# Kernel tuning notes

Measured on AMD Instinct MI355X. Metric: run time of the kernel, lower is better.

Reference implementation:

```python
import jax, jax.numpy as jnp
import numpy as np

N_NODES = 100000
N_EDGES = 640000
LATDIM = 128
GNN_LAYER = 3
LN_EPS = 1e-5


def setup_inputs() -> dict:
    key = jax.random.key(0)
    k1, k2, k3, k4 = jax.random.split(key, 4)
    embeds = jax.random.normal(k1, (N_NODES, LATDIM), dtype=jnp.float32)
    adj_row = jax.random.randint(k2, (N_EDGES,), 0, N_NODES, dtype=jnp.int32)
    adj_col = jax.random.randint(k3, (N_EDGES,), 0, N_NODES, dtype=jnp.int32)
    adj_val = jax.random.uniform(k4, (N_EDGES,), dtype=jnp.float32)
    return {"embeds": embeds, "adj_row": adj_row, "adj_col": adj_col, "adj_val": adj_val}


def _layer_norm(x):
    # nn.LayerNorm(latdim, elementwise_affine=False)
    mu = jnp.mean(x, axis=-1, keepdims=True)
    var = jnp.mean(jnp.square(x - mu), axis=-1, keepdims=True)
    return (x - mu) / jnp.sqrt(var + LN_EPS)


def _spmm(adj_row, adj_col, adj_val, x):
    # out[r] += val * x[c] for each edge (r, c, val)  -- sparse [N,N] @ [N,d]
    msgs = adj_val[:, None] * x[adj_col]  # [E, d]
    return jax.ops.segment_sum(msgs, adj_row, num_segments=N_NODES)


def reference(embeds, adj_row, adj_col, adj_val):
    x = _layer_norm(embeds)
    acc = jnp.zeros_like(x)  # gnn_layer > 0, so hop-0 embeds are NOT included
    for _ in range(GNN_LAYER):
        x = _spmm(adj_row, adj_col, adj_val, x)
        acc = acc + x
    return acc
```

## Files before the change

kernel.cpp:

```cpp
#include <hip/hip_runtime.h>

#define N_NODES 100000
#define N_EDGES 640000
#define LATDIM  128
#define LN_EPS  1e-5f

typedef unsigned int u32;
typedef float f32x4 __attribute__((ext_vector_type(4)));

#define SCAN_NB   98
#define N_PAD     (SCAN_NB * 1024)

#define LN_BLOCKS   (N_NODES / 8)
#define HIST_BLOCKS ((N_EDGES + 255) / 256)

#define APP_K      7
#define APP_EDGES  (256 * APP_K)
#define APP_NB     ((N_EDGES + APP_EDGES - 1) / APP_EDGES)

__device__ __forceinline__ float bflo(u32 u) { return __uint_as_float(u << 16); }
__device__ __forceinline__ float bfhi(u32 u) { return __uint_as_float(u & 0xffff0000u); }
__device__ __forceinline__ u32 pack_bf2(float a, float b) {
    u32 ua = __float_as_uint(a), ub = __float_as_uint(b);
    ua = (ua + 0x7fffu + ((ua >> 16) & 1u)) >> 16;
    ub = (ub + 0x7fffu + ((ub >> 16) & 1u)) >> 16;
    return ua | (ub << 16);
}

__device__ __forceinline__ u32 pack_edge(int col, float val) {
    u32 q = (u32)fminf(val * 32768.0f + 0.5f, 32767.0f);
    return (u32)col | (q << 17);
}
__device__ __forceinline__ int   edge_col(u32 r) { return (int)(r & 0x1FFFFu); }
__device__ __forceinline__ float edge_val(u32 r) { return (float)(r >> 17) * (1.0f / 32768.0f); }

__global__ __launch_bounds__(256) void ln_hist_kernel(const float* __restrict__ in,
                                                      u32* __restrict__ out,
                                                      const int* __restrict__ rowi,
                                                      int* __restrict__ cnt) {
    int b = blockIdx.x;
    if (b < LN_BLOCKS) {
        int tid  = threadIdx.x;
        int wave = tid >> 6;
        int lane = tid & 63;
        int half = lane >> 5;
        int sub  = lane & 31;
        int row  = b * 8 + wave * 2 + half;
        f32x4 v = __builtin_nontemporal_load(((const f32x4*)in) + (size_t)row * 32 + sub);
        float s  = v.x + v.y + v.z + v.w;
        float ss = v.x * v.x + v.y * v.y + v.z * v.z + v.w * v.w;
        #pragma unroll
        for (int o = 16; o > 0; o >>= 1) {
            s  += __shfl_xor(s,  o, 64);
            ss += __shfl_xor(ss, o, 64);
        }
        float mu   = s * (1.0f / LATDIM);
        float var  = ss * (1.0f / LATDIM) - mu * mu;
        float rstd = rsqrtf(var + LN_EPS);
        uint2 w;
        w.x = pack_bf2((v.x - mu) * rstd, (v.y - mu) * rstd);
        w.y = pack_bf2((v.z - mu) * rstd, (v.w - mu) * rstd);
        ((uint2*)out)[(size_t)row * 32 + sub] = w;
    } else {
        int e = (b - LN_BLOCKS) * 256 + threadIdx.x;
        if (e < N_EDGES) atomicAdd(&cnt[rowi[e]], 1);
    }
}

__global__ __launch_bounds__(256) void scan_a_kernel(int* __restrict__ cnt,
                                                     int* __restrict__ csums) {
    __shared__ int ts[256];
    int t = threadIdx.x;
    int base = blockIdx.x * 1024 + t * 4;
    int4 v = *(const int4*)(cnt + base);
    int s = v.x + v.y + v.z + v.w;
    ts[t] = s;
    __syncthreads();
    #pragma unroll
    for (int o = 1; o < 256; o <<= 1) {
        int u = 0;
        if (t >= o) u = ts[t - o];
        __syncthreads();
        if (t >= o) ts[t] += u;
        __syncthreads();
    }
    int excl = ts[t] - s;
    int4 w;
    w.x = excl;
    w.y = excl + v.x;
    w.z = excl + v.x + v.y;
    w.w = excl + v.x + v.y + v.z;
    *(int4*)(cnt + base) = w;
    if (t == 255) csums[blockIdx.x] = ts[255];
}

__global__ __launch_bounds__(128) void scan_b_kernel(const int* __restrict__ csums,
                                                     int* __restrict__ bsums,
                                                     int* __restrict__ gcur) {
    __shared__ int ss[128];
    int t = threadIdx.x;
    int own = (t < SCAN_NB) ? csums[t] : 0;
    ss[t] = own;
    __syncthreads();
    #pragma unroll
    for (int o = 1; o < 128; o <<= 1) {
        int u = 0;
        if (t >= o) u = ss[t - o];
        __syncthreads();
        if (t >= o) ss[t] += u;
        __syncthreads();
    }
    if (t < SCAN_NB) {
        int off = ss[t] - own;
        bsums[t] = off;
        gcur[t]  = off;
    }
    if (t == SCAN_NB) bsums[SCAN_NB] = N_EDGES;
}

__global__ __launch_bounds__(256) void bucket_append_kernel(const int* __restrict__ rowi,
                                                            const int* __restrict__ coli,
                                                            const float* __restrict__ vali,
                                                            int* __restrict__ gcur,
                                                            uint2* __restrict__ staging) {
    __shared__ int hist[SCAN_NB];
    __shared__ int base[SCAN_NB];
    int t = threadIdx.x;
    if (t < SCAN_NB) hist[t] = 0;
    __syncthreads();
    int e0 = blockIdx.x * APP_EDGES;
    int r[APP_K]; int c[APP_K]; float v[APP_K]; int bk[APP_K];
    #pragma unroll
    for (int k = 0; k < APP_K; ++k) {
        int e = e0 + k * 256 + t;
        if (e < N_EDGES) {
            r[k] = rowi[e]; c[k] = coli[e]; v[k] = vali[e];
            bk[k] = r[k] >> 10;
            atomicAdd(&hist[bk[k]], 1);
        } else {
            bk[k] = -1;
        }
    }
    __syncthreads();
    if (t < SCAN_NB) {
        int h = hist[t];
        base[t] = h ? atomicAdd(&gcur[t], h) : 0;
        hist[t] = 0;
    }
    __syncthreads();
    #pragma unroll
    for (int k = 0; k < APP_K; ++k) {
        if (bk[k] >= 0) {
            int idx = atomicAdd(&hist[bk[k]], 1);
            staging[base[bk[k]] + idx] =
                make_uint2(((u32)(r[k] & 1023) << 17) | (u32)c[k],
                           __float_as_uint(v[k]));
        }
    }
}

__global__ __launch_bounds__(256) void fine_scatter_kernel(const int* __restrict__ cnt,
                                                           const int* __restrict__ bsums,
                                                           const uint2* __restrict__ staging,
                                                           u32* __restrict__ recs) {
    __shared__ int cur[1024];
    int b = blockIdx.x, t = threadIdx.x;
    *(int4*)&cur[t * 4] = *(const int4*)&cnt[b * 1024 + t * 4];
    __syncthreads();
    int gbase = bsums[b];
    int n = bsums[b + 1] - gbase;
    for (int i = t; i < n; i += 256) {
        uint2 s = staging[gbase + i];
        int rowLocal = (int)(s.x >> 17);
        int col = (int)(s.x & 0x1FFFFu);
        int pos = gbase + atomicAdd(&cur[rowLocal], 1);
        recs[pos] = pack_edge(col, __uint_as_float(s.y));
    }
}

__global__ __launch_bounds__(256) void spmm_csr_kernel(const int* __restrict__ cnt,
                                                       const int* __restrict__ bsums,
                                                       const u32* __restrict__ recs,
                                                       const u32* __restrict__ x,
                                                       u32* __restrict__ y,
                                                       const u32* __restrict__ add0,
                                                       const u32* __restrict__ add1,
                                                       float* __restrict__ out,
                                                       int mode) {
    int tid  = threadIdx.x;
    int wave = tid >> 6;
    int lane = tid & 63;
    int row  = blockIdx.x * 16 + wave * 4 + (lane >> 4);
    int sub  = lane & 15;
    int e   = cnt[row]     + bsums[row >> 10];
    int end = cnt[row + 1] + bsums[(row + 1) >> 10];
    const uint4* x4 = (const uint4*)x;
    float a0=0,a1=0,a2=0,a3=0,a4=0,a5=0,a6=0,a7=0;
    for (; e + 4 <= end; e += 4) {
        u32 r0 = recs[e], r1 = recs[e+1], r2 = recs[e+2], r3 = recs[e+3];
        uint4 g0 = x4[(size_t)edge_col(r0) * 16 + sub];
        uint4 g1 = x4[(size_t)edge_col(r1) * 16 + sub];
        uint4 g2 = x4[(size_t)edge_col(r2) * 16 + sub];
        uint4 g3 = x4[(size_t)edge_col(r3) * 16 + sub];
        float v0 = edge_val(r0), v1 = edge_val(r1);
        float v2 = edge_val(r2), v3 = edge_val(r3);
        a0 += v0 * bflo(g0.x); a1 += v0 * bfhi(g0.x);
        a2 += v0 * bflo(g0.y); a3 += v0 * bfhi(g0.y);
        a4 += v0 * bflo(g0.z); a5 += v0 * bfhi(g0.z);
        a6 += v0 * bflo(g0.w); a7 += v0 * bfhi(g0.w);
        a0 += v1 * bflo(g1.x); a1 += v1 * bfhi(g1.x);
        a2 += v1 * bflo(g1.y); a3 += v1 * bfhi(g1.y);
        a4 += v1 * bflo(g1.z); a5 += v1 * bfhi(g1.z);
        a6 += v1 * bflo(g1.w); a7 += v1 * bfhi(g1.w);
        a0 += v2 * bflo(g2.x); a1 += v2 * bfhi(g2.x);
        a2 += v2 * bflo(g2.y); a3 += v2 * bfhi(g2.y);
        a4 += v2 * bflo(g2.z); a5 += v2 * bfhi(g2.z);
        a6 += v2 * bflo(g2.w); a7 += v2 * bfhi(g2.w);
        a0 += v3 * bflo(g3.x); a1 += v3 * bfhi(g3.x);
        a2 += v3 * bflo(g3.y); a3 += v3 * bfhi(g3.y);
        a4 += v3 * bflo(g3.z); a5 += v3 * bfhi(g3.z);
        a6 += v3 * bflo(g3.w); a7 += v3 * bfhi(g3.w);
    }
    for (; e < end; ++e) {
        u32 r = recs[e];
        uint4 g = x4[(size_t)edge_col(r) * 16 + sub];
        float v = edge_val(r);
        a0 += v * bflo(g.x); a1 += v * bfhi(g.x);
        a2 += v * bflo(g.y); a3 += v * bfhi(g.y);
        a4 += v * bflo(g.z); a5 += v * bfhi(g.z);
        a6 += v * bflo(g.w); a7 += v * bfhi(g.w);
    }
    size_t oi = (size_t)row * 16 + sub;
    if (mode == 2) {
        uint4 b0 = ((const uint4*)add0)[oi];
        uint4 b1 = ((const uint4*)add1)[oi];
        a0 += bflo(b0.x) + bflo(b1.x); a1 += bfhi(b0.x) + bfhi(b1.x);
        a2 += bflo(b0.y) + bflo(b1.y); a3 += bfhi(b0.y) + bfhi(b1.y);
        a4 += bflo(b0.z) + bflo(b1.z); a5 += bfhi(b0.z) + bfhi(b1.z);
        a6 += bflo(b0.w) + bflo(b1.w); a7 += bfhi(b0.w) + bfhi(b1.w);
        f32x4* o4 = (f32x4*)(out + (size_t)row * LATDIM + sub * 8);
        f32x4 q0 = {a0, a1, a2, a3};
        f32x4 q1 = {a4, a5, a6, a7};
        __builtin_nontemporal_store(q0, o4 + 0);
        __builtin_nontemporal_store(q1, o4 + 1);
    } else {
        uint4 w;
        w.x = pack_bf2(a0, a1);
        w.y = pack_bf2(a2, a3);
        w.z = pack_bf2(a4, a5);
        w.w = pack_bf2(a6, a7);
        ((uint4*)y)[oi] = w;
    }
}

__global__ __launch_bounds__(256) void ln_f32_kernel(const float* __restrict__ in,
                                                     float* __restrict__ out) {
    int tid  = threadIdx.x;
    int wave = tid >> 6;
    int lane = tid & 63;
    int half = lane >> 5;
    int sub  = lane & 31;
    int row  = blockIdx.x * 8 + wave * 2 + half;
    if (row >= N_NODES) return;
    float4 v = ((const float4*)in)[(size_t)row * 32 + sub];
    float s  = v.x + v.y + v.z + v.w;
    float ss = v.x * v.x + v.y * v.y + v.z * v.z + v.w * v.w;
    #pragma unroll
    for (int o = 16; o > 0; o >>= 1) {
        s  += __shfl_xor(s,  o, 64);
        ss += __shfl_xor(ss, o, 64);
    }
    float mu   = s * (1.0f / LATDIM);
    float var  = ss * (1.0f / LATDIM) - mu * mu;
    float rstd = rsqrtf(var + LN_EPS);
    float4 o4;
    o4.x = (v.x - mu) * rstd; o4.y = (v.y - mu) * rstd;
    o4.z = (v.z - mu) * rstd; o4.w = (v.w - mu) * rstd;
    ((float4*)out)[(size_t)row * 32 + sub] = o4;
}

__global__ __launch_bounds__(256) void spmm_atomic_kernel(const int* __restrict__ rowi,
                                                          const int* __restrict__ coli,
                                                          const float* __restrict__ vali,
                                                          const float* __restrict__ x,
                                                          float* __restrict__ y) {
    int t = blockIdx.x * 256 + threadIdx.x;
    int e = t >> 5;
    if (e >= N_EDGES) return;
    int k = t & 31;
    int r = rowi[e];
    int c = coli[e];
    float v = vali[e];
    float4 xv = ((const float4*)(x + (size_t)c * LATDIM))[k];
    float* yp = y + (size_t)r * LATDIM + k * 4;
    atomicAdd(yp + 0, v * xv.x);
    atomicAdd(yp + 1, v * xv.y);
    atomicAdd(yp + 2, v * xv.z);
    atomicAdd(yp + 3, v * xv.w);
}

__global__ __launch_bounds__(256) void addz_kernel(float* __restrict__ acc,
                                                   const float* __restrict__ x,
                                                   float* __restrict__ z,
                                                   int first) {
    size_t i = (size_t)blockIdx.x * 256 + threadIdx.x;
    float4 xv = ((const float4*)x)[i];
    float4* ap = ((float4*)acc) + i;
    if (first) {
        *ap = xv;
    } else {
        float4 a = *ap;
        a.x += xv.x; a.y += xv.y; a.z += xv.z; a.w += xv.w;
        *ap = a;
    }
    if (z) ((float4*)z)[i] = make_float4(0.f, 0.f, 0.f, 0.f);
}

extern "C" void kernel_launch(void* const* d_in, const int* in_sizes, int n_in,
                              void* d_out, int out_size, void* d_ws, size_t ws_size,
                              hipStream_t stream) {
    const float* embeds  = (const float*)d_in[0];
    const int*   adj_row = (const int*)d_in[1];
    const int*   adj_col = (const int*)d_in[2];
    const float* adj_val = (const float*)d_in[3];
    float* out = (float*)d_out;

    u32*   A16   = (u32*)d_ws;
    u32*   B16   = A16 + (size_t)N_NODES * (LATDIM / 2);
    int*   cnt   = (int*)(B16 + (size_t)N_NODES * (LATDIM / 2));
    int*   csums = cnt + N_PAD;
    int*   bsums = csums + 128;
    int*   gcur  = bsums + 128;
    uint2* staging = (uint2*)(gcur + 128);
    u32*   recs  = (u32*)(staging + N_EDGES);
    size_t need  = (size_t)((char*)(recs + N_EDGES) - (char*)d_ws);

    const int rowGrid = N_NODES / 16;

    if (ws_size >= need) {
        hipMemsetAsync(cnt, 0, (size_t)N_PAD * sizeof(int), stream);
        ln_hist_kernel<<<LN_BLOCKS + HIST_BLOCKS, 256, 0, stream>>>(embeds, A16,
                                                                    adj_row, cnt);
        scan_a_kernel<<<SCAN_NB, 256, 0, stream>>>(cnt, csums);
        scan_b_kernel<<<1, 128, 0, stream>>>(csums, bsums, gcur);
        bucket_append_kernel<<<APP_NB, 256, 0, stream>>>(adj_row, adj_col, adj_val,
                                                         gcur, staging);
        fine_scatter_kernel<<<SCAN_NB, 256, 0, stream>>>(cnt, bsums, staging, recs);
        spmm_csr_kernel<<<rowGrid, 256, 0, stream>>>(cnt, bsums, recs, A16, B16,
                                                     nullptr, nullptr, nullptr, 0);
        spmm_csr_kernel<<<rowGrid, 256, 0, stream>>>(cnt, bsums, recs, B16, A16,
                                                     nullptr, nullptr, nullptr, 0);
        spmm_csr_kernel<<<rowGrid, 256, 0, stream>>>(cnt, bsums, recs, A16, nullptr,
                                                     B16, A16, out, 2);
    } else {
        float* A = (float*)d_ws;
        float* B = A + (size_t)N_NODES * LATDIM;
        const size_t rowBytes = (size_t)N_NODES * LATDIM * sizeof(float);
        const int spmmGrid = (N_EDGES * 32 + 255) / 256;
        const int addGrid  = (N_NODES * LATDIM / 4 + 255) / 256;
        ln_f32_kernel<<<LN_BLOCKS, 256, 0, stream>>>(embeds, A);
        hipMemsetAsync(B, 0, rowBytes, stream);
        spmm_atomic_kernel<<<spmmGrid, 256, 0, stream>>>(adj_row, adj_col, adj_val, A, B);
        addz_kernel<<<addGrid, 256, 0, stream>>>(out, B, A, 1);
        spmm_atomic_kernel<<<spmmGrid, 256, 0, stream>>>(adj_row, adj_col, adj_val, B, A);
        addz_kernel<<<addGrid, 256, 0, stream>>>(out, A, B, 0);
        spmm_atomic_kernel<<<spmmGrid, 256, 0, stream>>>(adj_row, adj_col, adj_val, A, B);
        addz_kernel<<<addGrid, 256, 0, stream>>>(out, B, nullptr, 0);
    }
}
```

Baseline: 256.2 us.

## Replace global per-row histogram with per-bucket chunk counts and local fine scan

The global per-row atomic histogram, memset and two-level scan are replaced by per-block shared-memory histograms over 1024-row buckets, reduced by a single scan kernel. The per-row counts and exclusive offsets are then computed inside fine_scatter from the staged bucket data with a local scan, which also writes cnt for the SpMM. This removes a memset, one kernel launch and 640K global atomics, at the cost of reading the staging buffer twice in fine_scatter and a serial 100-entry loop in the scan kernel.

```diff
diff --git a/kernel.cpp b/kernel.cpp
--- a/kernel.cpp
+++ b/kernel.cpp
@@ -12,7 +12,9 @@
 #define N_PAD     (SCAN_NB * 1024)
 
 #define LN_BLOCKS   (N_NODES / 8)
-#define HIST_BLOCKS ((N_EDGES + 255) / 256)
+
+#define CNT_BLOCKS  100
+#define CNT_K       25
 
 #define APP_K      7
 #define APP_EDGES  (256 * APP_K)
@@ -34,18 +36,18 @@
 __device__ __forceinline__ int   edge_col(u32 r) { return (int)(r & 0x1FFFFu); }
 __device__ __forceinline__ float edge_val(u32 r) { return (float)(r >> 17) * (1.0f / 32768.0f); }
 
-__global__ __launch_bounds__(256) void ln_hist_kernel(const float* __restrict__ in,
-                                                      u32* __restrict__ out,
-                                                      const int* __restrict__ rowi,
-                                                      int* __restrict__ cnt) {
+__global__ __launch_bounds__(256) void ln_count_kernel(const float* __restrict__ in,
+                                                       u32* __restrict__ out,
+                                                       const int* __restrict__ rowi,
+                                                       int* __restrict__ partials) {
     int b = blockIdx.x;
-    if (b < LN_BLOCKS) {
+    if (b >= CNT_BLOCKS) {
         int tid  = threadIdx.x;
         int wave = tid >> 6;
         int lane = tid & 63;
         int half = lane >> 5;
         int sub  = lane & 31;
-        int row  = b * 8 + wave * 2 + half;
+        int row  = (b - CNT_BLOCKS) * 8 + wave * 2 + half;
         f32x4 v = __builtin_nontemporal_load(((const f32x4*)in) + (size_t)row * 32 + sub);
         float s  = v.x + v.y + v.z + v.w;
         float ss = v.x * v.x + v.y * v.y + v.z * v.z + v.w * v.w;
@@ -62,44 +64,30 @@
         w.y = pack_bf2((v.z - mu) * rstd, (v.w - mu) * rstd);
         ((uint2*)out)[(size_t)row * 32 + sub] = w;
     } else {
-        int e = (b - LN_BLOCKS) * 256 + threadIdx.x;
-        if (e < N_EDGES) atomicAdd(&cnt[rowi[e]], 1);
-    }
-}
-
-__global__ __launch_bounds__(256) void scan_a_kernel(int* __restrict__ cnt,
-                                                     int* __restrict__ csums) {
-    __shared__ int ts[256];
-    int t = threadIdx.x;
-    int base = blockIdx.x * 1024 + t * 4;
-    int4 v = *(const int4*)(cnt + base);
-    int s = v.x + v.y + v.z + v.w;
-    ts[t] = s;
-    __syncthreads();
-    #pragma unroll
-    for (int o = 1; o < 256; o <<= 1) {
-        int u = 0;
-        if (t >= o) u = ts[t - o];
-        __syncthreads();
-        if (t >= o) ts[t] += u;
-        __syncthreads();
-    }
-    int excl = ts[t] - s;
-    int4 w;
-    w.x = excl;
-    w.y = excl + v.x;
-    w.z = excl + v.x + v.y;
-    w.w = excl + v.x + v.y + v.z;
-    *(int4*)(cnt + base) = w;
-    if (t == 255) csums[blockIdx.x] = ts[255];
-}
-
-__global__ __launch_bounds__(128) void scan_b_kernel(const int* __restrict__ csums,
-                                                     int* __restrict__ bsums,
-                                                     int* __restrict__ gcur) {
+        __shared__ int hist[SCAN_NB];
+        int t = threadIdx.x;
+        if (t < SCAN_NB) hist[t] = 0;
+        __syncthreads();
+        int e0 = b * (256 * CNT_K);
+        #pragma unroll
+        for (int k = 0; k < CNT_K; ++k) {
+            int e = e0 + k * 256 + t;
+            atomicAdd(&hist[rowi[e] >> 10], 1);
+        }
+        __syncthreads();
+        if (t < SCAN_NB) partials[b * SCAN_NB + t] = hist[t];
+    }
+}
+
+__global__ __launch_bounds__(128) void scan_chunks_kernel(const int* __restrict__ partials,
+                                                          int* __restrict__ bsums,
+                                                          int* __restrict__ gcur) {
     __shared__ int ss[128];
     int t = threadIdx.x;
-    int own = (t < SCAN_NB) ? csums[t] : 0;
+    int own = 0;
+    if (t < SCAN_NB) {
+        for (int i = 0; i < CNT_BLOCKS; ++i) own += partials[i * SCAN_NB + t];
+    }
     ss[t] = own;
     __syncthreads();
     #pragma unroll
@@ -159,22 +147,49 @@
     }
 }
 
-__global__ __launch_bounds__(256) void fine_scatter_kernel(const int* __restrict__ cnt,
+__global__ __launch_bounds__(256) void fine_scatter_kernel(int* __restrict__ cnt,
                                                            const int* __restrict__ bsums,
                                                            const uint2* __restrict__ staging,
                                                            u32* __restrict__ recs) {
     __shared__ int cur[1024];
+    __shared__ int ts[256];
     int b = blockIdx.x, t = threadIdx.x;
-    *(int4*)&cur[t * 4] = *(const int4*)&cnt[b * 1024 + t * 4];
+    *(int4*)&cur[t * 4] = make_int4(0, 0, 0, 0);
     __syncthreads();
     int gbase = bsums[b];
     int n = bsums[b + 1] - gbase;
     for (int i = t; i < n; i += 256) {
         uint2 s = staging[gbase + i];
-        int rowLocal = (int)(s.x >> 17);
-        int col = (int)(s.x & 0x1FFFFu);
+        atomicAdd(&cur[s.x >> 17], 1);
+    }
+    __syncthreads();
+    int4 v = *(const int4*)&cur[t * 4];
+    int s = v.x + v.y + v.z + v.w;
+    ts[t] = s;
+    __syncthreads();
+    #pragma unroll
+    for (int o = 1; o < 256; o <<= 1) {
+        int u = 0;
+        if (t >= o) u = ts[t - o];
+        __syncthreads();
+        if (t >= o) ts[t] += u;
+        __syncthreads();
+    }
+    int excl = ts[t] - s;
+    int4 w;
+    w.x = excl;
+    w.y = excl + v.x;
+    w.z = excl + v.x + v.y;
+    w.w = excl + v.x + v.y + v.z;
+    *(int4*)&cnt[b * 1024 + t * 4] = w;
+    *(int4*)&cur[t * 4] = w;
+    __syncthreads();
+    for (int i = t; i < n; i += 256) {
+        uint2 s2 = staging[gbase + i];
+        int rowLocal = (int)(s2.x >> 17);
+        int col = (int)(s2.x & 0x1FFFFu);
         int pos = gbase + atomicAdd(&cur[rowLocal], 1);
-        recs[pos] = pack_edge(col, __uint_as_float(s.y));
+        recs[pos] = pack_edge(col, __uint_as_float(s2.y));
     }
 }
 
@@ -328,8 +343,8 @@
     u32*   A16   = (u32*)d_ws;
     u32*   B16   = A16 + (size_t)N_NODES * (LATDIM / 2);
     int*   cnt   = (int*)(B16 + (size_t)N_NODES * (LATDIM / 2));
-    int*   csums = cnt + N_PAD;
-    int*   bsums = csums + 128;
+    int*   partials = cnt + N_PAD;
+    int*   bsums = partials + CNT_BLOCKS * SCAN_NB;
     int*   gcur  = bsums + 128;
     uint2* staging = (uint2*)(gcur + 128);
     u32*   recs  = (u32*)(staging + N_EDGES);
@@ -338,11 +353,9 @@
     const int rowGrid = N_NODES / 16;
 
     if (ws_size >= need) {
-        hipMemsetAsync(cnt, 0, (size_t)N_PAD * sizeof(int), stream);
-        ln_hist_kernel<<<LN_BLOCKS + HIST_BLOCKS, 256, 0, stream>>>(embeds, A16,
-                                                                    adj_row, cnt);
-        scan_a_kernel<<<SCAN_NB, 256, 0, stream>>>(cnt, csums);
-        scan_b_kernel<<<1, 128, 0, stream>>>(csums, bsums, gcur);
+        ln_count_kernel<<<CNT_BLOCKS + LN_BLOCKS, 256, 0, stream>>>(embeds, A16,
+                                                                    adj_row, partials);
+        scan_chunks_kernel<<<1, 128, 0, stream>>>(partials, bsums, gcur);
         bucket_append_kernel<<<APP_NB, 256, 0, stream>>>(adj_row, adj_col, adj_val,
                                                          gcur, staging);
         fine_scatter_kernel<<<SCAN_NB, 256, 0, stream>>>(cnt, bsums, staging, recs);
```

After: 240.5 us, median of 2. 6.1% less time.
